# Optimization experiments

Hardware: AMD Instinct MI355X
Metric: run time of the kernel (lower is better)

## Reference

```python
import jax, jax.numpy as jnp
import numpy as np

B, C_IN, C_OUT, E, K = 4, 32, 64, 200000, 5


def setup_inputs() -> dict:
    key = jax.random.key(0)
    k1, k2, k3, k4 = jax.random.split(key, 4)
    x = jax.random.normal(k1, (B, C_IN, E), dtype=jnp.float32)
    # Gi: per-edge [self_id, n1, n2, n3, n4] one-ring indices into the edge axis
    Gi = jax.random.randint(k2, (B, E, K), 0, E, dtype=jnp.int32)
    # Conv2d(C_IN, C_OUT, kernel_size=(1, K)) weights, PyTorch layout (O, I, 1, K)
    fan_in = C_IN * K
    bound = 1.0 / np.sqrt(fan_in)
    W = jax.random.uniform(k3, (C_OUT, C_IN, 1, K), jnp.float32, -bound, bound)
    b = jax.random.uniform(k4, (C_OUT,), jnp.float32, -bound, bound)
    return {"x": x, "Gi": Gi, "W": W, "b": b}


def _mesh_conv(x, Gi, W, b):
    Bn, C, En = x.shape
    # prepend zero-padding column (index 0 after Gi+1 maps to zeros)
    xp = jnp.concatenate([jnp.zeros((Bn, C, 1), x.dtype), x], axis=2)  # (B, C, E+1)
    idx = Gi.astype(jnp.int32) + 1  # (B, E, 5)
    # gather 1-ring neighbor features: f[b, c, e, j] = xp[b, c, idx[b, e, j]]
    f = jax.vmap(lambda xb, ib: xb[:, ib])(xp, idx)  # (B, C, E, 5)
    f0, f1, f2, f3, f4 = (f[..., j] for j in range(5))
    # symmetric, order-invariant combine
    G = jnp.stack([f0, f1 + f3, f2 + f4, jnp.abs(f1 - f3), jnp.abs(f2 - f4)], axis=3)
    # Conv2d with kernel (1, K), no padding -> contraction over (C_in, K)
    out = jnp.einsum('bcek,ock->boe', G, W[:, :, 0, :]) + b[None, :, None]
    return out[..., None]  # (B, C_out, E, 1)


def reference(x, Gi, W, b):
    return _mesh_conv(x, Gi, W, b)
```

## Files before the change

kernel.cpp:

```cpp
#include <hip/hip_runtime.h>

typedef unsigned int u32;
typedef __bf16 bf16x8 __attribute__((ext_vector_type(8)));
typedef float f32x4 __attribute__((ext_vector_type(4)));

#define B_DIM 4
#define E_DIM 200000
#define C_OUT 64
#define TPB   12500
#define NT    (B_DIM * TPB)
#define NBLK  1280
#define WLDS_U4 1792

__device__ __forceinline__ u32 pack_bf2(float lo, float hi) {
  u32 a = __float_as_uint(lo) + 0x8000u;
  u32 b = __float_as_uint(hi) + 0x8000u;
  return __builtin_amdgcn_perm(b, a, 0x07060302u);
}

__device__ __forceinline__ u32 absdiff_pack(u32 a, u32 b) {
  float alo = __uint_as_float(a << 16), ahi = __uint_as_float(a & 0xffff0000u);
  float blo = __uint_as_float(b << 16), bhi = __uint_as_float(b & 0xffff0000u);
  u32 dlo = __float_as_uint(alo - blo) + 0x8000u;
  u32 dhi = __float_as_uint(ahi - bhi) + 0x8000u;
  return __builtin_amdgcn_perm(dhi, dlo, 0x07060302u) & 0x7fff7fffu;
}

__device__ __forceinline__ uint4 absdiff_vec(uint4 a, uint4 b) {
  return make_uint4(absdiff_pack(a.x, b.x), absdiff_pack(a.y, b.y),
                    absdiff_pack(a.z, b.z), absdiff_pack(a.w, b.w));
}

__global__ __launch_bounds__(256) void xpose_kernel(const float* __restrict__ x,
                                                    u32* __restrict__ xT) {
  __shared__ u32 T[256 * 17];
  const int b = blockIdx.y;
  const int e0 = blockIdx.x * 256;
  const int t = threadIdx.x;
  const int nrows = min(256, E_DIM - e0);
  const float* xb = x + (size_t)b * 32 * E_DIM + e0;
  if (t < nrows) {
#pragma unroll
    for (int u = 0; u < 16; ++u) {
      const float lo = xb[(size_t)(2 * u) * E_DIM + t];
      const float hi = xb[(size_t)(2 * u + 1) * E_DIM + t];
      T[t * 17 + u] = pack_bf2(lo, hi);
    }
  }
  __syncthreads();
  const int total = nrows * 16;
  u32* dst = xT + ((size_t)b * E_DIM + e0) * 16;
#pragma unroll
  for (int k = 0; k < 16; ++k) {
    const int g = t + k * 256;
    if (g < total) dst[g] = T[(g >> 4) * 17 + (g & 15)];
  }
}

__global__ __launch_bounds__(256) void prep_w(const float* __restrict__ W,
                                              u32* __restrict__ Wa2) {
  const int p = blockIdx.x * 256 + threadIdx.x;
  if (p >= 7168) return;
  const int r = p & 3;
  const int o = (p >> 2) & 63;
  const int q = (p >> 8) & 3;
  const int s = p >> 10;
  const int kmap[7] = {0, 1, 2, 1, 2, 3, 4};
  const int c0 = q * 8 + 2 * r;
  const float w0 = W[(o * 32 + c0) * 5 + kmap[s]];
  const float w1 = W[(o * 32 + c0 + 1) * 5 + kmap[s]];
  Wa2[p] = pack_bf2(w0, w1);
}

__global__ __launch_bounds__(256) void mesh_main(const u32* __restrict__ xT,
                                                 const int* __restrict__ Gi,
                                                 const u32* __restrict__ Wa2,
                                                 const float* __restrict__ bias,
                                                 float* __restrict__ out) {
  __shared__ uint4 Wl[WLDS_U4];
  {
    const uint4* src = (const uint4*)Wa2;
#pragma unroll
    for (int k = 0; k < 7; ++k) Wl[threadIdx.x + k * 256] = src[threadIdx.x + k * 256];
  }
  __syncthreads();

  const int l = threadIdx.x & 63;
  const int wv = threadIdx.x >> 6;
  const int n = l & 15;
  const int q = l >> 4;
  const int NW = NBLK * 4;

  f32x4 bv[4];
#pragma unroll
  for (int og = 0; og < 4; ++og) bv[og] = *(const f32x4*)(bias + og * 16 + q * 4);

  const uint4* xb4 = (const uint4*)xT;

  int t = blockIdx.x * 4 + wv;

  int gcur[5], gnext[5];
  {
    const int b = t / TPB;
    const int e = (t - b * TPB) * 16 + n;
    const int* gp = Gi + (b * E_DIM + e) * 5;
#pragma unroll
    for (int s = 0; s < 5; ++s) gcur[s] = b * E_DIM + gp[s];
  }
  uint4 cur[5];
#pragma unroll
  for (int s = 0; s < 5; ++s) cur[s] = xb4[(size_t)gcur[s] * 4 + q];

  int t1 = t + NW;
  if (t1 < NT) {
    const int b = t1 / TPB;
    const int e = (t1 - b * TPB) * 16 + n;
    const int* gp = Gi + (b * E_DIM + e) * 5;
#pragma unroll
    for (int s = 0; s < 5; ++s) gnext[s] = b * E_DIM + gp[s];
  }

  for (;;) {
    const bool has = t1 < NT;
    uint4 nxt[5];
    if (has) {
#pragma unroll
      for (int s = 0; s < 5; ++s) nxt[s] = xb4[(size_t)gnext[s] * 4 + q];
    }
    const int t2 = t1 + NW;
    if (t2 < NT) {
      const int b = t2 / TPB;
      const int e = (t2 - b * TPB) * 16 + n;
      const int* gp = Gi + (b * E_DIM + e) * 5;
#pragma unroll
      for (int s = 0; s < 5; ++s) gnext[s] = b * E_DIM + gp[s];
    }

    union { uint4 u; bf16x8 v; } frag[7];
#pragma unroll
    for (int s = 0; s < 5; ++s) frag[s].u = cur[s];
    frag[5].u = absdiff_vec(cur[1], cur[3]);
    frag[6].u = absdiff_vec(cur[2], cur[4]);

    f32x4 acc0 = bv[0], acc1 = bv[1], acc2 = bv[2], acc3 = bv[3];
#pragma unroll
    for (int c = 0; c < 7; ++c) {
      const uint4* wp = Wl + (c * 4 + q) * 64 + n;
      union { uint4 u; bf16x8 v; } a0, a1, a2, a3;
      a0.u = wp[0];
      a1.u = wp[16];
      a2.u = wp[32];
      a3.u = wp[48];
      acc0 = __builtin_amdgcn_mfma_f32_16x16x32_bf16(a0.v, frag[c].v, acc0, 0, 0, 0);
      acc1 = __builtin_amdgcn_mfma_f32_16x16x32_bf16(a1.v, frag[c].v, acc1, 0, 0, 0);
      acc2 = __builtin_amdgcn_mfma_f32_16x16x32_bf16(a2.v, frag[c].v, acc2, 0, 0, 0);
      acc3 = __builtin_amdgcn_mfma_f32_16x16x32_bf16(a3.v, frag[c].v, acc3, 0, 0, 0);
    }

    {
      const int b = t / TPB;
      const int e0 = (t - b * TPB) * 16;
      float* ob = out + ((size_t)(b * C_OUT + q * 4) * E_DIM + e0 + n);
#pragma unroll
      for (int r = 0; r < 4; ++r) {
        ob[(size_t)(0 * 16 + r) * E_DIM] = acc0[r];
        ob[(size_t)(1 * 16 + r) * E_DIM] = acc1[r];
        ob[(size_t)(2 * 16 + r) * E_DIM] = acc2[r];
        ob[(size_t)(3 * 16 + r) * E_DIM] = acc3[r];
      }
    }

    if (!has) break;
    t = t1;
    t1 = t2;
#pragma unroll
    for (int s = 0; s < 5; ++s) cur[s] = nxt[s];
  }
}

extern "C" void kernel_launch(void* const* d_in, const int* in_sizes, int n_in,
                              void* d_out, int out_size, void* d_ws, size_t ws_size,
                              hipStream_t stream) {
  const float* x    = (const float*)d_in[0];
  const int*   Gi   = (const int*)d_in[1];
  const float* W    = (const float*)d_in[2];
  const float* bias = (const float*)d_in[3];
  float* out = (float*)d_out;

  u32* xT  = (u32*)d_ws;
  u32* Wa2 = xT + (size_t)B_DIM * E_DIM * 16;

  dim3 gx((E_DIM + 255) / 256, B_DIM);
  xpose_kernel<<<gx, 256, 0, stream>>>(x, xT);

  prep_w<<<28, 256, 0, stream>>>(W, Wa2);

  mesh_main<<<NBLK, 256, 0, stream>>>(xT, Gi, Wa2, bias, out);
}
```

Baseline: 390.4 us.

## Fuse transpose, weight prep and mesh conv into one cooperative kernel

Merges the x transpose/bf16 pack, the weight packing and the main gather+MFMA kernel into a single cooperative launch that uses a grid-wide sync between the transpose phase and the gather phase. Each block packs the weights straight into LDS instead of reading a pre-packed buffer. This removes two extra kernel launches and their inter-kernel gaps. In exchange, the transpose now writes uint4 rows per thread without the LDS staging, and the grid is capped at the cooperative occupancy limit, with a fallback to the old three-kernel path if the launch fails.

Measured after the change: 433.7 us. 11.1% more time.

```diff
diff --git a/kernel.cpp b/kernel.cpp
--- a/kernel.cpp
+++ b/kernel.cpp
@@ -1,4 +1,5 @@
 #include <hip/hip_runtime.h>
+#include <hip/hip_cooperative_groups.h>
 
 typedef unsigned int u32;
 typedef __bf16 bf16x8 __attribute__((ext_vector_type(8)));
@@ -10,6 +11,8 @@
 #define TPB   12500
 #define NT    (B_DIM * TPB)
 #define NBLK  1280
+#define ECH   782
+#define NCHUNK (B_DIM * ECH)
 #define WLDS_U4 1792
 
 __device__ __forceinline__ u32 pack_bf2(float lo, float hi) {
@@ -31,71 +34,56 @@
                     absdiff_pack(a.z, b.z), absdiff_pack(a.w, b.w));
 }
 
-__global__ __launch_bounds__(256) void xpose_kernel(const float* __restrict__ x,
-                                                    u32* __restrict__ xT) {
-  __shared__ u32 T[256 * 17];
-  const int b = blockIdx.y;
-  const int e0 = blockIdx.x * 256;
-  const int t = threadIdx.x;
-  const int nrows = min(256, E_DIM - e0);
-  const float* xb = x + (size_t)b * 32 * E_DIM + e0;
-  if (t < nrows) {
-#pragma unroll
-    for (int u = 0; u < 16; ++u) {
-      const float lo = xb[(size_t)(2 * u) * E_DIM + t];
-      const float hi = xb[(size_t)(2 * u + 1) * E_DIM + t];
-      T[t * 17 + u] = pack_bf2(lo, hi);
-    }
-  }
-  __syncthreads();
-  const int total = nrows * 16;
-  u32* dst = xT + ((size_t)b * E_DIM + e0) * 16;
-#pragma unroll
-  for (int k = 0; k < 16; ++k) {
-    const int g = t + k * 256;
-    if (g < total) dst[g] = T[(g >> 4) * 17 + (g & 15)];
-  }
-}
-
-__global__ __launch_bounds__(256) void prep_w(const float* __restrict__ W,
-                                              u32* __restrict__ Wa2) {
-  const int p = blockIdx.x * 256 + threadIdx.x;
-  if (p >= 7168) return;
-  const int r = p & 3;
-  const int o = (p >> 2) & 63;
-  const int q = (p >> 8) & 3;
-  const int s = p >> 10;
-  const int kmap[7] = {0, 1, 2, 1, 2, 3, 4};
-  const int c0 = q * 8 + 2 * r;
-  const float w0 = W[(o * 32 + c0) * 5 + kmap[s]];
-  const float w1 = W[(o * 32 + c0 + 1) * 5 + kmap[s]];
-  Wa2[p] = pack_bf2(w0, w1);
-}
-
-__global__ __launch_bounds__(256) void mesh_main(const u32* __restrict__ xT,
-                                                 const int* __restrict__ Gi,
-                                                 const u32* __restrict__ Wa2,
-                                                 const float* __restrict__ bias,
-                                                 float* __restrict__ out) {
+__global__ __launch_bounds__(256) void fused_mesh(
+    const float* __restrict__ x, const int* __restrict__ Gi,
+    const float* __restrict__ W, const float* __restrict__ bias,
+    u32* __restrict__ xT, float* __restrict__ out, int nblk) {
   __shared__ uint4 Wl[WLDS_U4];
+
   {
-    const uint4* src = (const uint4*)Wa2;
-#pragma unroll
-    for (int k = 0; k < 7; ++k) Wl[threadIdx.x + k * 256] = src[threadIdx.x + k * 256];
-  }
-  __syncthreads();
-
-  const int l = threadIdx.x & 63;
-  const int wv = threadIdx.x >> 6;
+    u32* wl = (u32*)&Wl[0];
+#pragma unroll
+    for (int k = 0; k < 28; ++k) {
+      const int p = (int)threadIdx.x + k * 256;
+      const int r = p & 3;
+      const int o = (p >> 2) & 63;
+      const int q = (p >> 8) & 3;
+      const int s = p >> 10;
+      const int kk = s < 3 ? s : s - 2;
+      const int c0 = q * 8 + 2 * r;
+      const float w0 = W[(o * 32 + c0) * 5 + kk];
+      const float w1 = W[(o * 32 + c0 + 1) * 5 + kk];
+      wl[p] = pack_bf2(w0, w1);
+    }
+  }
+
+  for (int cid = blockIdx.x; cid < NCHUNK; cid += nblk) {
+    const int b = cid / ECH;
+    const int e = (cid - b * ECH) * 256 + (int)threadIdx.x;
+    if (e < E_DIM) {
+      const float* xb = x + (size_t)b * 32 * E_DIM + e;
+      uint4 row[4];
+#pragma unroll
+      for (int u = 0; u < 16; ++u) {
+        const float lo = xb[(size_t)(2 * u) * E_DIM];
+        const float hi = xb[(size_t)(2 * u + 1) * E_DIM];
+        ((u32*)row)[u] = pack_bf2(lo, hi);
+      }
+      uint4* dst = (uint4*)(xT + ((size_t)b * E_DIM + e) * 16);
+#pragma unroll
+      for (int k = 0; k < 4; ++k) dst[k] = row[k];
+    }
+  }
+
+  const int l = (int)threadIdx.x & 63;
+  const int wv = (int)threadIdx.x >> 6;
   const int n = l & 15;
   const int q = l >> 4;
-  const int NW = NBLK * 4;
+  const int NW = nblk * 4;
 
   f32x4 bv[4];
 #pragma unroll
   for (int og = 0; og < 4; ++og) bv[og] = *(const f32x4*)(bias + og * 16 + q * 4);
-
-  const uint4* xb4 = (const uint4*)xT;
 
   int t = blockIdx.x * 4 + wv;
 
@@ -107,10 +95,6 @@
 #pragma unroll
     for (int s = 0; s < 5; ++s) gcur[s] = b * E_DIM + gp[s];
   }
-  uint4 cur[5];
-#pragma unroll
-  for (int s = 0; s < 5; ++s) cur[s] = xb4[(size_t)gcur[s] * 4 + q];
-
   int t1 = t + NW;
   if (t1 < NT) {
     const int b = t1 / TPB;
@@ -119,6 +103,13 @@
 #pragma unroll
     for (int s = 0; s < 5; ++s) gnext[s] = b * E_DIM + gp[s];
   }
+
+  cooperative_groups::this_grid().sync();
+
+  const uint4* xb4 = (const uint4*)xT;
+  uint4 cur[5];
+#pragma unroll
+  for (int s = 0; s < 5; ++s) cur[s] = xb4[(size_t)gcur[s] * 4 + q];
 
   for (;;) {
     const bool has = t1 < NT;
@@ -178,6 +169,152 @@
   }
 }
 
+__global__ __launch_bounds__(256) void xpose_kernel(const float* __restrict__ x,
+                                                    u32* __restrict__ xT) {
+  __shared__ u32 T[256 * 17];
+  const int b = blockIdx.y;
+  const int e0 = blockIdx.x * 256;
+  const int t = threadIdx.x;
+  const int nrows = min(256, E_DIM - e0);
+  const float* xb = x + (size_t)b * 32 * E_DIM + e0;
+  if (t < nrows) {
+#pragma unroll
+    for (int u = 0; u < 16; ++u) {
+      const float lo = xb[(size_t)(2 * u) * E_DIM + t];
+      const float hi = xb[(size_t)(2 * u + 1) * E_DIM + t];
+      T[t * 17 + u] = pack_bf2(lo, hi);
+    }
+  }
+  __syncthreads();
+  const int total = nrows * 16;
+  u32* dst = xT + ((size_t)b * E_DIM + e0) * 16;
+#pragma unroll
+  for (int k = 0; k < 16; ++k) {
+    const int g = t + k * 256;
+    if (g < total) dst[g] = T[(g >> 4) * 17 + (g & 15)];
+  }
+}
+
+__global__ __launch_bounds__(256) void prep_w(const float* __restrict__ W,
+                                              u32* __restrict__ Wa2) {
+  const int p = blockIdx.x * 256 + threadIdx.x;
+  if (p >= 7168) return;
+  const int r = p & 3;
+  const int o = (p >> 2) & 63;
+  const int q = (p >> 8) & 3;
+  const int s = p >> 10;
+  const int kk = s < 3 ? s : s - 2;
+  const int c0 = q * 8 + 2 * r;
+  const float w0 = W[(o * 32 + c0) * 5 + kk];
+  const float w1 = W[(o * 32 + c0 + 1) * 5 + kk];
+  Wa2[p] = pack_bf2(w0, w1);
+}
+
+__global__ __launch_bounds__(256) void mesh_main(const u32* __restrict__ xT,
+                                                 const int* __restrict__ Gi,
+                                                 const u32* __restrict__ Wa2,
+                                                 const float* __restrict__ bias,
+                                                 float* __restrict__ out) {
+  __shared__ uint4 Wl[WLDS_U4];
+  {
+    const uint4* src = (const uint4*)Wa2;
+#pragma unroll
+    for (int k = 0; k < 7; ++k) Wl[threadIdx.x + k * 256] = src[threadIdx.x + k * 256];
+  }
+  __syncthreads();
+
+  const int l = threadIdx.x & 63;
+  const int wv = threadIdx.x >> 6;
+  const int n = l & 15;
+  const int q = l >> 4;
+  const int NW = NBLK * 4;
+
+  f32x4 bv[4];
+#pragma unroll
+  for (int og = 0; og < 4; ++og) bv[og] = *(const f32x4*)(bias + og * 16 + q * 4);
+
+  const uint4* xb4 = (const uint4*)xT;
+  int t = blockIdx.x * 4 + wv;
+
+  int gcur[5], gnext[5];
+  {
+    const int b = t / TPB;
+    const int e = (t - b * TPB) * 16 + n;
+    const int* gp = Gi + (b * E_DIM + e) * 5;
+#pragma unroll
+    for (int s = 0; s < 5; ++s) gcur[s] = b * E_DIM + gp[s];
+  }
+  uint4 cur[5];
+#pragma unroll
+  for (int s = 0; s < 5; ++s) cur[s] = xb4[(size_t)gcur[s] * 4 + q];
+
+  int t1 = t + NW;
+  if (t1 < NT) {
+    const int b = t1 / TPB;
+    const int e = (t1 - b * TPB) * 16 + n;
+    const int* gp = Gi + (b * E_DIM + e) * 5;
+#pragma unroll
+    for (int s = 0; s < 5; ++s) gnext[s] = b * E_DIM + gp[s];
+  }
+
+  for (;;) {
+    const bool has = t1 < NT;
+    uint4 nxt[5];
+    if (has) {
+#pragma unroll
+      for (int s = 0; s < 5; ++s) nxt[s] = xb4[(size_t)gnext[s] * 4 + q];
+    }
+    const int t2 = t1 + NW;
+    if (t2 < NT) {
+      const int b = t2 / TPB;
+      const int e = (t2 - b * TPB) * 16 + n;
+      const int* gp = Gi + (b * E_DIM + e) * 5;
+#pragma unroll
+      for (int s = 0; s < 5; ++s) gnext[s] = b * E_DIM + gp[s];
+    }
+
+    union { uint4 u; bf16x8 v; } frag[7];
+#pragma unroll
+    for (int s = 0; s < 5; ++s) frag[s].u = cur[s];
+    frag[5].u = absdiff_vec(cur[1], cur[3]);
+    frag[6].u = absdiff_vec(cur[2], cur[4]);
+
+    f32x4 acc0 = bv[0], acc1 = bv[1], acc2 = bv[2], acc3 = bv[3];
+#pragma unroll
+    for (int c = 0; c < 7; ++c) {
+      const uint4* wp = Wl + (c * 4 + q) * 64 + n;
+      union { uint4 u; bf16x8 v; } a0, a1, a2, a3;
+      a0.u = wp[0];
+      a1.u = wp[16];
+      a2.u = wp[32];
+      a3.u = wp[48];
+      acc0 = __builtin_amdgcn_mfma_f32_16x16x32_bf16(a0.v, frag[c].v, acc0, 0, 0, 0);
+      acc1 = __builtin_amdgcn_mfma_f32_16x16x32_bf16(a1.v, frag[c].v, acc1, 0, 0, 0);
+      acc2 = __builtin_amdgcn_mfma_f32_16x16x32_bf16(a2.v, frag[c].v, acc2, 0, 0, 0);
+      acc3 = __builtin_amdgcn_mfma_f32_16x16x32_bf16(a3.v, frag[c].v, acc3, 0, 0, 0);
+    }
+
+    {
+      const int b = t / TPB;
+      const int e0 = (t - b * TPB) * 16;
+      float* ob = out + ((size_t)(b * C_OUT + q * 4) * E_DIM + e0 + n);
+#pragma unroll
+      for (int r = 0; r < 4; ++r) {
+        ob[(size_t)(0 * 16 + r) * E_DIM] = acc0[r];
+        ob[(size_t)(1 * 16 + r) * E_DIM] = acc1[r];
+        ob[(size_t)(2 * 16 + r) * E_DIM] = acc2[r];
+        ob[(size_t)(3 * 16 + r) * E_DIM] = acc3[r];
+      }
+    }
+
+    if (!has) break;
+    t = t1;
+    t1 = t2;
+#pragma unroll
+    for (int s = 0; s < 5; ++s) cur[s] = nxt[s];
+  }
+}
+
 extern "C" void kernel_launch(void* const* d_in, const int* in_sizes, int n_in,
                               void* d_out, int out_size, void* d_ws, size_t ws_size,
                               hipStream_t stream) {
@@ -187,13 +324,37 @@
   const float* bias = (const float*)d_in[3];
   float* out = (float*)d_out;
 
-  u32* xT  = (u32*)d_ws;
-  u32* Wa2 = xT + (size_t)B_DIM * E_DIM * 16;
-
-  dim3 gx((E_DIM + 255) / 256, B_DIM);
-  xpose_kernel<<<gx, 256, 0, stream>>>(x, xT);
-
-  prep_w<<<28, 256, 0, stream>>>(W, Wa2);
-
-  mesh_main<<<NBLK, 256, 0, stream>>>(xT, Gi, Wa2, bias, out);
-}
+  u32* xT = (u32*)d_ws;
+
+  static int maxb = -2;
+  if (maxb == -2) {
+    int mb = 0;
+    if (hipOccupancyMaxActiveBlocksPerMultiprocessor(&mb, fused_mesh, 256, 0) != hipSuccess)
+      mb = 0;
+    maxb = mb;
+  }
+
+  bool done = false;
+  if (maxb >= 1) {
+    int nblk = maxb * 256;
+    if (nblk > NBLK) nblk = NBLK;
+    const float* xa = x; const int* ga = Gi; const float* wa = W;
+    const float* ba = bias; u32* xta = xT; float* oa = out; int nb = nblk;
+    void* args[] = {&xa, &ga, &wa, &ba, &xta, &oa, &nb};
+    hipError_t err = hipLaunchCooperativeKernel((const void*)fused_mesh,
+                                                dim3(nblk), dim3(256), args, 0, stream);
+    if (err == hipSuccess) {
+      done = true;
+    } else {
+      (void)hipGetLastError();
+    }
+  }
+
+  if (!done) {
+    u32* Wa2 = xT + (size_t)B_DIM * E_DIM * 16;
+    dim3 gx((E_DIM + 255) / 256, B_DIM);
+    xpose_kernel<<<gx, 256, 0, stream>>>(x, xT);
+    prep_w<<<28, 256, 0, stream>>>(W, Wa2);
+    mesh_main<<<NBLK, 256, 0, stream>>>(xT, Gi, Wa2, bias, out);
+  }
+}
```

## Deepen gather prefetch to two tiles and fold weight prep into main kernel

Applied to the files above, without the earlier changes.

The main loop now keeps two tiles of gathered neighbour features in flight plus prefetched indices for a third, instead of one tile ahead. This is meant to hide more of the random-gather latency. The separate weight-packing kernel is removed: each block packs bf16 weights and bias into LDS itself, which saves a launch but repeats global reads per block. Grid size drops to 1024 blocks, launch bounds are raised to 4 blocks per CU, and bias moves into LDS. The deeper prefetch adds register pressure.

Result: slower. 590.5 us (+51.2%).

```diff
diff --git a/kernel.cpp b/kernel.cpp
--- a/kernel.cpp
+++ b/kernel.cpp
@@ -9,7 +9,8 @@
 #define C_OUT 64
 #define TPB   12500
 #define NT    (B_DIM * TPB)
-#define NBLK  1280
+#define NBLK  1024
+#define NW    (NBLK * 4)
 #define WLDS_U4 1792
 
 __device__ __forceinline__ u32 pack_bf2(float lo, float hi) {
@@ -57,109 +58,121 @@
   }
 }
 
-__global__ __launch_bounds__(256) void prep_w(const float* __restrict__ W,
-                                              u32* __restrict__ Wa2) {
-  const int p = blockIdx.x * 256 + threadIdx.x;
-  if (p >= 7168) return;
-  const int r = p & 3;
-  const int o = (p >> 2) & 63;
-  const int q = (p >> 8) & 3;
-  const int s = p >> 10;
-  const int kmap[7] = {0, 1, 2, 1, 2, 3, 4};
-  const int c0 = q * 8 + 2 * r;
-  const float w0 = W[(o * 32 + c0) * 5 + kmap[s]];
-  const float w1 = W[(o * 32 + c0 + 1) * 5 + kmap[s]];
-  Wa2[p] = pack_bf2(w0, w1);
-}
-
-__global__ __launch_bounds__(256) void mesh_main(const u32* __restrict__ xT,
-                                                 const int* __restrict__ Gi,
-                                                 const u32* __restrict__ Wa2,
-                                                 const float* __restrict__ bias,
-                                                 float* __restrict__ out) {
+__global__ __launch_bounds__(256, 4) void mesh_main(const u32* __restrict__ xT,
+                                                    const int* __restrict__ Gi,
+                                                    const float* __restrict__ W,
+                                                    const float* __restrict__ bias,
+                                                    float* __restrict__ out) {
   __shared__ uint4 Wl[WLDS_U4];
-  {
-    const uint4* src = (const uint4*)Wa2;
-#pragma unroll
-    for (int k = 0; k < 7; ++k) Wl[threadIdx.x + k * 256] = src[threadIdx.x + k * 256];
+  __shared__ float Bl[64];
+
+  {
+    u32* wl = (u32*)&Wl[0];
+#pragma unroll
+    for (int k = 0; k < 28; ++k) {
+      const int p = (int)threadIdx.x + k * 256;
+      const int r = p & 3;
+      const int o = (p >> 2) & 63;
+      const int qq = (p >> 8) & 3;
+      const int s = p >> 10;
+      const int kk = s < 3 ? s : s - 2;
+      const int c0 = qq * 8 + 2 * r;
+      const float w0 = W[(o * 32 + c0) * 5 + kk];
+      const float w1 = W[(o * 32 + c0 + 1) * 5 + kk];
+      wl[p] = pack_bf2(w0, w1);
+    }
+    if (threadIdx.x < 64) Bl[threadIdx.x] = bias[threadIdx.x];
   }
   __syncthreads();
 
-  const int l = threadIdx.x & 63;
-  const int wv = threadIdx.x >> 6;
+  const int l = (int)threadIdx.x & 63;
+  const int wv = (int)threadIdx.x >> 6;
   const int n = l & 15;
   const int q = l >> 4;
-  const int NW = NBLK * 4;
-
-  f32x4 bv[4];
-#pragma unroll
-  for (int og = 0; og < 4; ++og) bv[og] = *(const f32x4*)(bias + og * 16 + q * 4);
 
   const uint4* xb4 = (const uint4*)xT;
-
-  int t = blockIdx.x * 4 + wv;
-
-  int gcur[5], gnext[5];
-  {
-    const int b = t / TPB;
-    const int e = (t - b * TPB) * 16 + n;
+  int t0 = blockIdx.x * 4 + wv;
+
+  int idxn[5];
+  uint4 g0[5], g1[5];
+  {
+    const int b = t0 / TPB;
+    const int e = (t0 - b * TPB) * 16 + n;
     const int* gp = Gi + (b * E_DIM + e) * 5;
-#pragma unroll
-    for (int s = 0; s < 5; ++s) gcur[s] = b * E_DIM + gp[s];
-  }
-  uint4 cur[5];
-#pragma unroll
-  for (int s = 0; s < 5; ++s) cur[s] = xb4[(size_t)gcur[s] * 4 + q];
-
-  int t1 = t + NW;
-  if (t1 < NT) {
+    int ia[5];
+#pragma unroll
+    for (int s = 0; s < 5; ++s) ia[s] = b * E_DIM + gp[s];
+#pragma unroll
+    for (int s = 0; s < 5; ++s) g0[s] = xb4[(size_t)ia[s] * 4 + q];
+  }
+  {
+    const int t1 = t0 + NW;
     const int b = t1 / TPB;
     const int e = (t1 - b * TPB) * 16 + n;
     const int* gp = Gi + (b * E_DIM + e) * 5;
-#pragma unroll
-    for (int s = 0; s < 5; ++s) gnext[s] = b * E_DIM + gp[s];
+    int ib[5];
+#pragma unroll
+    for (int s = 0; s < 5; ++s) ib[s] = b * E_DIM + gp[s];
+#pragma unroll
+    for (int s = 0; s < 5; ++s) g1[s] = xb4[(size_t)ib[s] * 4 + q];
+  }
+  {
+    const int t2 = t0 + 2 * NW;
+    const int b = t2 / TPB;
+    const int e = (t2 - b * TPB) * 16 + n;
+    const int* gp = Gi + (b * E_DIM + e) * 5;
+#pragma unroll
+    for (int s = 0; s < 5; ++s) idxn[s] = b * E_DIM + gp[s];
   }
 
   for (;;) {
-    const bool has = t1 < NT;
-    uint4 nxt[5];
-    if (has) {
-#pragma unroll
-      for (int s = 0; s < 5; ++s) nxt[s] = xb4[(size_t)gnext[s] * 4 + q];
-    }
-    const int t2 = t1 + NW;
-    if (t2 < NT) {
-      const int b = t2 / TPB;
-      const int e = (t2 - b * TPB) * 16 + n;
+    const bool has1 = (t0 + NW) < NT;
+    const bool has2 = (t0 + 2 * NW) < NT;
+
+    uint4 g2[5];
+    if (has2) {
+#pragma unroll
+      for (int s = 0; s < 5; ++s) g2[s] = xb4[(size_t)idxn[s] * 4 + q];
+    }
+    const int t3 = t0 + 3 * NW;
+    if (t3 < NT) {
+      const int b = t3 / TPB;
+      const int e = (t3 - b * TPB) * 16 + n;
       const int* gp = Gi + (b * E_DIM + e) * 5;
 #pragma unroll
-      for (int s = 0; s < 5; ++s) gnext[s] = b * E_DIM + gp[s];
-    }
-
-    union { uint4 u; bf16x8 v; } frag[7];
-#pragma unroll
-    for (int s = 0; s < 5; ++s) frag[s].u = cur[s];
-    frag[5].u = absdiff_vec(cur[1], cur[3]);
-    frag[6].u = absdiff_vec(cur[2], cur[4]);
-
-    f32x4 acc0 = bv[0], acc1 = bv[1], acc2 = bv[2], acc3 = bv[3];
+      for (int s = 0; s < 5; ++s) idxn[s] = b * E_DIM + gp[s];
+    }
+
+    union U { uint4 u; bf16x8 v; };
+    U f5, f6;
+    f5.u = absdiff_vec(g0[1], g0[3]);
+    f6.u = absdiff_vec(g0[2], g0[4]);
+
+    f32x4 acc0 = *(const f32x4*)&Bl[0 * 16 + q * 4];
+    f32x4 acc1 = *(const f32x4*)&Bl[1 * 16 + q * 4];
+    f32x4 acc2 = *(const f32x4*)&Bl[2 * 16 + q * 4];
+    f32x4 acc3 = *(const f32x4*)&Bl[3 * 16 + q * 4];
 #pragma unroll
     for (int c = 0; c < 7; ++c) {
+      U fr;
+      if (c < 5) fr.u = g0[c];
+      else if (c == 5) fr = f5;
+      else fr = f6;
       const uint4* wp = Wl + (c * 4 + q) * 64 + n;
-      union { uint4 u; bf16x8 v; } a0, a1, a2, a3;
+      U a0, a1;
       a0.u = wp[0];
       a1.u = wp[16];
-      a2.u = wp[32];
-      a3.u = wp[48];
-      acc0 = __builtin_amdgcn_mfma_f32_16x16x32_bf16(a0.v, frag[c].v, acc0, 0, 0, 0);
-      acc1 = __builtin_amdgcn_mfma_f32_16x16x32_bf16(a1.v, frag[c].v, acc1, 0, 0, 0);
-      acc2 = __builtin_amdgcn_mfma_f32_16x16x32_bf16(a2.v, frag[c].v, acc2, 0, 0, 0);
-      acc3 = __builtin_amdgcn_mfma_f32_16x16x32_bf16(a3.v, frag[c].v, acc3, 0, 0, 0);
+      acc0 = __builtin_amdgcn_mfma_f32_16x16x32_bf16(a0.v, fr.v, acc0, 0, 0, 0);
+      acc1 = __builtin_amdgcn_mfma_f32_16x16x32_bf16(a1.v, fr.v, acc1, 0, 0, 0);
+      a0.u = wp[32];
+      a1.u = wp[48];
+      acc2 = __builtin_amdgcn_mfma_f32_16x16x32_bf16(a0.v, fr.v, acc2, 0, 0, 0);
+      acc3 = __builtin_amdgcn_mfma_f32_16x16x32_bf16(a1.v, fr.v, acc3, 0, 0, 0);
     }
 
     {
-      const int b = t / TPB;
-      const int e0 = (t - b * TPB) * 16;
+      const int b = t0 / TPB;
+      const int e0 = (t0 - b * TPB) * 16;
       float* ob = out + ((size_t)(b * C_OUT + q * 4) * E_DIM + e0 + n);
 #pragma unroll
       for (int r = 0; r < 4; ++r) {
@@ -170,11 +183,10 @@
       }
     }
 
-    if (!has) break;
-    t = t1;
-    t1 = t2;
-#pragma unroll
-    for (int s = 0; s < 5; ++s) cur[s] = nxt[s];
+    if (!has1) break;
+    t0 += NW;
+#pragma unroll
+    for (int s = 0; s < 5; ++s) { g0[s] = g1[s]; g1[s] = g2[s]; }
   }
 }
 
@@ -187,13 +199,10 @@
   const float* bias = (const float*)d_in[3];
   float* out = (float*)d_out;
 
-  u32* xT  = (u32*)d_ws;
-  u32* Wa2 = xT + (size_t)B_DIM * E_DIM * 16;
+  u32* xT = (u32*)d_ws;
 
   dim3 gx((E_DIM + 255) / 256, B_DIM);
   xpose_kernel<<<gx, 256, 0, stream>>>(x, xT);
 
-  prep_w<<<28, 256, 0, stream>>>(W, Wa2);
-
-  mesh_main<<<NBLK, 256, 0, stream>>>(xT, Gi, Wa2, bias, out);
-}
+  mesh_main<<<NBLK, 256, 0, stream>>>(xT, Gi, W, bias, out);
+}
```

## Fold weight packing into main kernel, drop prep launch, shrink grid

Applied to the files above, without the earlier changes.

Removes the separate prep_w launch. Each block of the main kernel now packs the bf16 weights from the raw fp32 W into LDS itself. Bias moves to LDS and is read each iteration instead of being held in registers, and the weight fragments reuse two registers to lower register pressure. The grid shrinks from 1280 to 1024 blocks. This saves a kernel launch, at the cost of redundant per-block weight packing and strided global reads of W.

New measurement: 404.4 us. 3.6% more time.

```diff
diff --git a/kernel.cpp b/kernel.cpp
--- a/kernel.cpp
+++ b/kernel.cpp
@@ -9,7 +9,8 @@
 #define C_OUT 64
 #define TPB   12500
 #define NT    (B_DIM * TPB)
-#define NBLK  1280
+#define NBLK  1024
+#define NW    (NBLK * 4)
 #define WLDS_U4 1792
 
 __device__ __forceinline__ u32 pack_bf2(float lo, float hi) {
@@ -57,43 +58,37 @@
   }
 }
 
-__global__ __launch_bounds__(256) void prep_w(const float* __restrict__ W,
-                                              u32* __restrict__ Wa2) {
-  const int p = blockIdx.x * 256 + threadIdx.x;
-  if (p >= 7168) return;
-  const int r = p & 3;
-  const int o = (p >> 2) & 63;
-  const int q = (p >> 8) & 3;
-  const int s = p >> 10;
-  const int kmap[7] = {0, 1, 2, 1, 2, 3, 4};
-  const int c0 = q * 8 + 2 * r;
-  const float w0 = W[(o * 32 + c0) * 5 + kmap[s]];
-  const float w1 = W[(o * 32 + c0 + 1) * 5 + kmap[s]];
-  Wa2[p] = pack_bf2(w0, w1);
-}
-
 __global__ __launch_bounds__(256) void mesh_main(const u32* __restrict__ xT,
                                                  const int* __restrict__ Gi,
-                                                 const u32* __restrict__ Wa2,
+                                                 const float* __restrict__ W,
                                                  const float* __restrict__ bias,
                                                  float* __restrict__ out) {
   __shared__ uint4 Wl[WLDS_U4];
+  __shared__ float Bl[64];
+
   {
-    const uint4* src = (const uint4*)Wa2;
+    u32* wl = (u32*)&Wl[0];
 #pragma unroll
-    for (int k = 0; k < 7; ++k) Wl[threadIdx.x + k * 256] = src[threadIdx.x + k * 256];
+    for (int k = 0; k < 28; ++k) {
+      const int p = (int)threadIdx.x + k * 256;
+      const int r = p & 3;
+      const int o = (p >> 2) & 63;
+      const int qq = (p >> 8) & 3;
+      const int s = p >> 10;
+      const int kk = s < 3 ? s : s - 2;
+      const int c0 = qq * 8 + 2 * r;
+      const float w0 = W[(o * 32 + c0) * 5 + kk];
+      const float w1 = W[(o * 32 + c0 + 1) * 5 + kk];
+      wl[p] = pack_bf2(w0, w1);
+    }
+    if (threadIdx.x < 64) Bl[threadIdx.x] = bias[threadIdx.x];
   }
   __syncthreads();
 
-  const int l = threadIdx.x & 63;
-  const int wv = threadIdx.x >> 6;
+  const int l = (int)threadIdx.x & 63;
+  const int wv = (int)threadIdx.x >> 6;
   const int n = l & 15;
   const int q = l >> 4;
-  const int NW = NBLK * 4;
-
-  f32x4 bv[4];
-#pragma unroll
-  for (int og = 0; og < 4; ++og) bv[og] = *(const f32x4*)(bias + og * 16 + q * 4);
 
   const uint4* xb4 = (const uint4*)xT;
 
@@ -136,25 +131,29 @@
       for (int s = 0; s < 5; ++s) gnext[s] = b * E_DIM + gp[s];
     }
 
-    union { uint4 u; bf16x8 v; } frag[7];
+    union U { uint4 u; bf16x8 v; };
+    U frag[7];
 #pragma unroll
     for (int s = 0; s < 5; ++s) frag[s].u = cur[s];
     frag[5].u = absdiff_vec(cur[1], cur[3]);
     frag[6].u = absdiff_vec(cur[2], cur[4]);
 
-    f32x4 acc0 = bv[0], acc1 = bv[1], acc2 = bv[2], acc3 = bv[3];
+    f32x4 acc0 = *(const f32x4*)&Bl[0 * 16 + q * 4];
+    f32x4 acc1 = *(const f32x4*)&Bl[1 * 16 + q * 4];
+    f32x4 acc2 = *(const f32x4*)&Bl[2 * 16 + q * 4];
+    f32x4 acc3 = *(const f32x4*)&Bl[3 * 16 + q * 4];
 #pragma unroll
     for (int c = 0; c < 7; ++c) {
       const uint4* wp = Wl + (c * 4 + q) * 64 + n;
-      union { uint4 u; bf16x8 v; } a0, a1, a2, a3;
+      U a0, a1;
       a0.u = wp[0];
       a1.u = wp[16];
-      a2.u = wp[32];
-      a3.u = wp[48];
       acc0 = __builtin_amdgcn_mfma_f32_16x16x32_bf16(a0.v, frag[c].v, acc0, 0, 0, 0);
       acc1 = __builtin_amdgcn_mfma_f32_16x16x32_bf16(a1.v, frag[c].v, acc1, 0, 0, 0);
-      acc2 = __builtin_amdgcn_mfma_f32_16x16x32_bf16(a2.v, frag[c].v, acc2, 0, 0, 0);
-      acc3 = __builtin_amdgcn_mfma_f32_16x16x32_bf16(a3.v, frag[c].v, acc3, 0, 0, 0);
+      a0.u = wp[32];
+      a1.u = wp[48];
+      acc2 = __builtin_amdgcn_mfma_f32_16x16x32_bf16(a0.v, frag[c].v, acc2, 0, 0, 0);
+      acc3 = __builtin_amdgcn_mfma_f32_16x16x32_bf16(a1.v, frag[c].v, acc3, 0, 0, 0);
     }
 
     {
@@ -187,13 +186,10 @@
   const float* bias = (const float*)d_in[3];
   float* out = (float*)d_out;
 
-  u32* xT  = (u32*)d_ws;
-  u32* Wa2 = xT + (size_t)B_DIM * E_DIM * 16;
+  u32* xT = (u32*)d_ws;
 
   dim3 gx((E_DIM + 255) / 256, B_DIM);
   xpose_kernel<<<gx, 256, 0, stream>>>(x, xT);
 
-  prep_w<<<28, 256, 0, stream>>>(W, Wa2);
-
-  mesh_main<<<NBLK, 256, 0, stream>>>(xT, Gi, Wa2, bias, out);
+  mesh_main<<<NBLK, 256, 0, stream>>>(xT, Gi, W, bias, out);
 }
```
